# Kernel optimization log

Hardware: AMD Instinct MI355X
Metric: run time of the kernel (lower is better)

The kernel has to match this reference:

```python
import jax, jax.numpy as jnp
import numpy as np

P = 1.0  # Yager t-norm exponent (tnorm_p)


def _patches(x, k):
    # x: [B, C, H, W] -> [B, C*k*k, Ho, Wo], feature ordering (c, kh, kw) like torch unfold
    B, C, H, W = x.shape
    Ho, Wo = H - k + 1, W - k + 1
    cols = [x[:, :, i:i + Ho, j:j + Wo] for i in range(k) for j in range(k)]
    p = jnp.stack(cols, axis=2)  # [B, C, k*k, Ho, Wo]
    return p.reshape(B, C * k * k, Ho, Wo)


def _max_yager2d(x, w, p):
    # Fuzzy conv: Yager t-norm T(a,b)=max(0, 1-((1-a)^p+(1-b)^p)^(1/p)) between each
    # patch element and kernel weight, aggregated with max over the receptive field.
    O, C, k, _ = w.shape
    pat = _patches(x, k)                       # [B, L, Ho, Wo], L = C*k*k
    wf = w.reshape(O, -1)                      # [O, L]
    a = 1.0 - pat[:, None]                     # [B, 1, L, Ho, Wo]
    b = 1.0 - wf[None, :, :, None, None]       # [1, O, L, 1, 1]
    t = jnp.maximum(0.0, 1.0 - (a ** p + b ** p) ** (1.0 / p))
    return jnp.max(t, axis=2)                  # [B, O, Ho, Wo]


def _maxpool2(x):
    return jax.lax.reduce_window(x, -jnp.inf, jax.lax.max,
                                 (1, 1, 2, 2), (1, 1, 2, 2), 'VALID')


def setup_inputs() -> dict:
    key = jax.random.key(0)
    k1, k2, k3, k4, k5, k6, k7 = jax.random.split(key, 7)
    B = 128
    inputs = jax.random.uniform(k1, (B, 3, 32, 32), dtype=jnp.float32)
    # fuzzy kernels are membership values in [0,1]
    w1 = jax.random.uniform(k2, (6, 3, 5, 5), dtype=jnp.float32)
    w2 = jax.random.uniform(k3, (16, 6, 5, 5), dtype=jnp.float32)
    w3 = jax.random.uniform(k4, (120, 16, 5, 5), dtype=jnp.float32)
    wd = jax.random.normal(k5, (120, 84), dtype=jnp.float32) * 0.1  # DenseDefuzzy weights
    wf = jax.random.normal(k6, (84, 10), dtype=jnp.float32) * 0.1   # fc5 weight
    bf = jax.random.normal(k7, (10,), dtype=jnp.float32) * 0.01     # fc5 bias
    return {"inputs": inputs, "w1": w1, "w2": w2, "w3": w3,
            "wd": wd, "wf": wf, "bf": bf}


def reference(inputs, w1, w2, w3, wd, wf, bf):
    x = _maxpool2(_max_yager2d(inputs, w1, P))   # [B,6,14,14]
    x = _maxpool2(_max_yager2d(x, w2, P))        # [B,16,5,5]
    x = _max_yager2d(x, w3, P)                   # [B,120,1,1]
    x = x.reshape(x.shape[0], -1)                # [B,120]
    x = jnp.tanh(x @ wd)                         # DenseDefuzzy (unnormalized) + tanh
    return jax.nn.log_softmax(x @ wf + bf, axis=-1)
```

## Files before the change

kernel.cpp:

```cpp
#include <hip/hip_runtime.h>
#include <math.h>


#define NT 512
#define ROWS 34
#define PLANE (32 * ROWS)

__global__ __launch_bounds__(NT) void fused_lenet(
    const float* __restrict__ x,
    const float* __restrict__ w1,
    const float* __restrict__ w2,
    const float* __restrict__ w3,
    const float* __restrict__ wd,
    const float* __restrict__ wf,
    const float* __restrict__ bfv,
    float* __restrict__ out)
{
    const int img = blockIdx.x;
    const int tid = threadIdx.x;

    __shared__ float s_in[3 * PLANE];
    __shared__ float s_w1r[450];
    __shared__ float s_w2r[2400];
    __shared__ float s_w1d[648];
    __shared__ float s_w2d[3456];
    __shared__ unsigned s_a1u[1176];
    __shared__ unsigned s_a2u[400];
    __shared__ float s_a3[120];
    __shared__ float s_a4[84];

    {
        const float2* src = (const float2*)(x + img * 3072);
        for (int i = tid; i < 1536; i += NT) {
            const int c = i >> 9, rem = i & 511, r = rem >> 4, col2 = rem & 15;
            ((float2*)s_in)[c * (PLANE / 2) + r * (ROWS / 2) + col2] = src[i];
        }
        for (int i = tid; i < 225; i += NT)
            ((float2*)s_w1r)[i] = ((const float2*)w1)[i];
        for (int i = tid; i < 1200; i += NT)
            ((float2*)s_w2r)[i] = ((const float2*)w2)[i];
        for (int i = tid; i < 1176; i += NT) s_a1u[i] = 0u;
        if (tid < 400) s_a2u[tid] = 0u;
    }
    __syncthreads();

    for (int e = tid; e < 4104; e += NT) {
        const float* raw;
        float* dst;
        int v;
        if (e < 648) {
            const int oc = e / 108, u = e - oc * 108;
            const int c = u / 36; v = u - c * 36;
            raw = s_w1r + (oc * 3 + c) * 25;
            dst = s_w1d + e;
        } else {
            const int idx = e - 648;
            const int oc = idx / 216, u = idx - oc * 216;
            const int c = u / 36; v = u - c * 36;
            raw = s_w2r + (oc * 6 + c) * 25;
            dst = s_w2d + idx;
        }
        const int r = v / 6, col = v - r * 6;
        float m = -1e30f;
        #pragma unroll
        for (int dy = 0; dy < 2; ++dy) {
            const int kh = r - dy;
            if ((unsigned)kh > 4u) continue;
            #pragma unroll
            for (int dx = 0; dx < 2; ++dx) {
                const int kw = col - dx;
                if ((unsigned)kw > 4u) continue;
                m = fmaxf(m, raw[kh * 5 + kw]);
            }
        }
        *dst = m;
    }
    __syncthreads();

    if (tid < 504) {
        const int c = tid / 168;
        const int rr = tid - c * 168;
        const int oc = rr / 28;
        const int r2 = rr - oc * 28;
        const int py = r2 >> 1, s = r2 & 1;
        float acc[7];
        #pragma unroll
        for (int j = 0; j < 7; ++j) acc[j] = -1e30f;
        const float* wbase = s_w1d + (oc * 3 + c) * 36;
        #pragma unroll
        for (int uy = 0; uy < 6; ++uy) {
            const float* xr = s_in + c * PLANE + (2 * py + uy) * ROWS + 14 * s;
            float xv[18];
            #pragma unroll
            for (int i2 = 0; i2 < 9; ++i2)
                ((float2*)xv)[i2] = ((const float2*)xr)[i2];
            float wv[6];
            #pragma unroll
            for (int i2 = 0; i2 < 3; ++i2)
                ((float2*)wv)[i2] = ((const float2*)(wbase + uy * 6))[i2];
            #pragma unroll
            for (int j = 0; j < 7; ++j) {
                #pragma unroll
                for (int ux = 0; ux < 6; ++ux)
                    acc[j] = fmaxf(acc[j], xv[2 * j + ux] + wv[ux]);
            }
        }
        const int obase = oc * 196 + py * 14 + 7 * s;
        #pragma unroll
        for (int j = 0; j < 7; ++j) {
            const float rl = fmaxf(acc[j] - 1.0f, 0.0f);
            atomicMax(&s_a1u[obase + j], __float_as_uint(rl));
        }
    }
    __syncthreads();

    if (tid < 480) {
        const int oc = tid / 30;
        const int rr = tid - oc * 30;
        const int py = rr / 6;
        const int c = rr - py * 6;
        float acc[5];
        #pragma unroll
        for (int j = 0; j < 5; ++j) acc[j] = -1e30f;
        const float* a1f = (const float*)s_a1u;
        const float* wbase = s_w2d + (oc * 6 + c) * 36;
        #pragma unroll
        for (int uy = 0; uy < 6; ++uy) {
            const float* xr = a1f + c * 196 + (2 * py + uy) * 14;
            float xv[14];
            #pragma unroll
            for (int i2 = 0; i2 < 7; ++i2)
                ((float2*)xv)[i2] = ((const float2*)xr)[i2];
            float wv[6];
            #pragma unroll
            for (int i2 = 0; i2 < 3; ++i2)
                ((float2*)wv)[i2] = ((const float2*)(wbase + uy * 6))[i2];
            #pragma unroll
            for (int j = 0; j < 5; ++j) {
                #pragma unroll
                for (int ux = 0; ux < 6; ++ux)
                    acc[j] = fmaxf(acc[j], xv[2 * j + ux] + wv[ux]);
            }
        }
        const int obase = oc * 25 + py * 5;
        #pragma unroll
        for (int j = 0; j < 5; ++j) {
            const float rl = fmaxf(acc[j] - 1.0f, 0.0f);
            atomicMax(&s_a2u[obase + j], __float_as_uint(rl));
        }
    }
    __syncthreads();

    if (tid < 480) {
        const int o = tid >> 2, q = tid & 3;
        const float4* wv = (const float4*)(w3 + o * 400 + q * 100);
        const float4* av = (const float4*)((const float*)s_a2u + q * 100);
        float m = -1e30f;
        #pragma unroll 5
        for (int l = 0; l < 25; ++l) {
            const float4 w = wv[l];
            const float4 a = av[l];
            m = fmaxf(m, fmaxf(fmaxf(a.x + w.x, a.y + w.y),
                               fmaxf(a.z + w.z, a.w + w.w)));
        }
        m = fmaxf(m, __shfl_xor(m, 1));
        m = fmaxf(m, __shfl_xor(m, 2));
        if (q == 0) s_a3[o] = fmaxf(m - 1.0f, 0.0f);
    }
    __syncthreads();

    if (tid < 336) {
        const int o = tid >> 2, q = tid & 3;
        float acc = 0.0f;
        #pragma unroll 6
        for (int i = 0; i < 30; ++i) {
            const int k = q * 30 + i;
            acc = fmaf(s_a3[k], wd[k * 84 + o], acc);
        }
        acc += __shfl_xor(acc, 1);
        acc += __shfl_xor(acc, 2);
        if (q == 0) s_a4[o] = tanhf(acc);
    }
    __syncthreads();

    if (tid < 64) {
        float acc = 0.0f;
        if (tid < 40) {
            const int o = tid >> 2, q = tid & 3;
            #pragma unroll 7
            for (int i = 0; i < 21; ++i) {
                const int k = q * 21 + i;
                acc = fmaf(s_a4[k], wf[k * 10 + o], acc);
            }
            acc += __shfl_xor(acc, 1);
            acc += __shfl_xor(acc, 2);
            acc += bfv[o];
        }
        const float lg = __shfl(acc, (tid < 10) ? tid * 4 : 0);
        if (tid < 16) {
            float v = (tid < 10) ? lg : -1e30f;
            #pragma unroll
            for (int d = 1; d < 16; d <<= 1)
                v = fmaxf(v, __shfl_xor(v, d));
            float e = (tid < 10) ? expf(lg - v) : 0.0f;
            float ssum = e;
            #pragma unroll
            for (int d = 1; d < 16; d <<= 1)
                ssum += __shfl_xor(ssum, d);
            if (tid < 10)
                out[img * 10 + tid] = lg - v - logf(ssum);
        }
    }
}

extern "C" void kernel_launch(void* const* d_in, const int* in_sizes, int n_in,
                              void* d_out, int out_size, void* d_ws, size_t ws_size,
                              hipStream_t stream) {
    const float* x   = (const float*)d_in[0];
    const float* w1  = (const float*)d_in[1];
    const float* w2  = (const float*)d_in[2];
    const float* w3  = (const float*)d_in[3];
    const float* wd  = (const float*)d_in[4];
    const float* wf  = (const float*)d_in[5];
    const float* bfv = (const float*)d_in[6];
    float* out = (float*)d_out;

    const int B = in_sizes[0] / (3 * 32 * 32);
    fused_lenet<<<dim3(B), dim3(NT), 0, stream>>>(
        x, w1, w2, w3, wd, wf, bfv, out);
}
```

Before: 84.68 us.

## Double block size and split conv rows across thread halves, load weights directly

Raises threads per block from 512 to 1024. Conv1 and conv2 now split each dilated-weight window's six rows into two halves of three, handled by separate threads, and combine them through the existing shared-memory atomicMax. Conv3 and the dense layer split their reductions over 8 lanes instead of 4. The raw weights are read from global memory during dilation, which drops the staging copy and one barrier. The cost is more atomics and heavier register limits at 1024 threads, which may lower occupancy with only 128 blocks.

```diff
diff --git a/kernel.cpp b/kernel.cpp
--- a/kernel.cpp
+++ b/kernel.cpp
@@ -2,7 +2,7 @@
 #include <math.h>
 
 
-#define NT 512
+#define NT 1024
 #define ROWS 34
 #define PLANE (32 * ROWS)
 
@@ -20,8 +20,6 @@
     const int tid = threadIdx.x;
 
     __shared__ float s_in[3 * PLANE];
-    __shared__ float s_w1r[450];
-    __shared__ float s_w2r[2400];
     __shared__ float s_w1d[648];
     __shared__ float s_w2d[3456];
     __shared__ unsigned s_a1u[1176];
@@ -35,61 +33,59 @@
             const int c = i >> 9, rem = i & 511, r = rem >> 4, col2 = rem & 15;
             ((float2*)s_in)[c * (PLANE / 2) + r * (ROWS / 2) + col2] = src[i];
         }
-        for (int i = tid; i < 225; i += NT)
-            ((float2*)s_w1r)[i] = ((const float2*)w1)[i];
-        for (int i = tid; i < 1200; i += NT)
-            ((float2*)s_w2r)[i] = ((const float2*)w2)[i];
         for (int i = tid; i < 1176; i += NT) s_a1u[i] = 0u;
         if (tid < 400) s_a2u[tid] = 0u;
-    }
-    __syncthreads();
-
-    for (int e = tid; e < 4104; e += NT) {
-        const float* raw;
-        float* dst;
-        int v;
-        if (e < 648) {
-            const int oc = e / 108, u = e - oc * 108;
-            const int c = u / 36; v = u - c * 36;
-            raw = s_w1r + (oc * 3 + c) * 25;
-            dst = s_w1d + e;
-        } else {
-            const int idx = e - 648;
-            const int oc = idx / 216, u = idx - oc * 216;
-            const int c = u / 36; v = u - c * 36;
-            raw = s_w2r + (oc * 6 + c) * 25;
-            dst = s_w2d + idx;
-        }
-        const int r = v / 6, col = v - r * 6;
-        float m = -1e30f;
-        #pragma unroll
-        for (int dy = 0; dy < 2; ++dy) {
-            const int kh = r - dy;
-            if ((unsigned)kh > 4u) continue;
-            #pragma unroll
-            for (int dx = 0; dx < 2; ++dx) {
-                const int kw = col - dx;
-                if ((unsigned)kw > 4u) continue;
-                m = fmaxf(m, raw[kh * 5 + kw]);
-            }
-        }
-        *dst = m;
-    }
-    __syncthreads();
-
-    if (tid < 504) {
-        const int c = tid / 168;
-        const int rr = tid - c * 168;
-        const int oc = rr / 28;
-        const int r2 = rr - oc * 28;
-        const int py = r2 >> 1, s = r2 & 1;
+
+        for (int e = tid; e < 4104; e += NT) {
+            const float* raw;
+            float* dst;
+            int v;
+            if (e < 648) {
+                const int oc = e / 108, u = e - oc * 108;
+                const int c = u / 36; v = u - c * 36;
+                raw = w1 + (oc * 3 + c) * 25;
+                dst = s_w1d + e;
+            } else {
+                const int idx = e - 648;
+                const int oc = idx / 216, u = idx - oc * 216;
+                const int c = u / 36; v = u - c * 36;
+                raw = w2 + (oc * 6 + c) * 25;
+                dst = s_w2d + idx;
+            }
+            const int r = v / 6, col = v - r * 6;
+            float m = -1e30f;
+            #pragma unroll
+            for (int dy = 0; dy < 2; ++dy) {
+                const int kh = r - dy;
+                if ((unsigned)kh > 4u) continue;
+                #pragma unroll
+                for (int dx = 0; dx < 2; ++dx) {
+                    const int kw = col - dx;
+                    if ((unsigned)kw > 4u) continue;
+                    m = fmaxf(m, raw[kh * 5 + kw]);
+                }
+            }
+            *dst = m;
+        }
+    }
+    __syncthreads();
+
+    if (tid < 1008) {
+        const int c = tid / 336;
+        const int rr = tid - c * 336;
+        const int oc = rr / 56;
+        const int r2 = rr - oc * 56;
+        const int py = r2 >> 2;
+        const int s = (r2 >> 1) & 1;
+        const int h = r2 & 1;
         float acc[7];
         #pragma unroll
         for (int j = 0; j < 7; ++j) acc[j] = -1e30f;
-        const float* wbase = s_w1d + (oc * 3 + c) * 36;
-        #pragma unroll
-        for (int uy = 0; uy < 6; ++uy) {
-            const float* xr = s_in + c * PLANE + (2 * py + uy) * ROWS + 14 * s;
+        const float* wbase = s_w1d + (oc * 3 + c) * 36 + h * 18;
+        const float* xbase = s_in + c * PLANE + (2 * py + 3 * h) * ROWS + 14 * s;
+        #pragma unroll
+        for (int u = 0; u < 3; ++u) {
+            const float* xr = xbase + u * ROWS;
             float xv[18];
             #pragma unroll
             for (int i2 = 0; i2 < 9; ++i2)
@@ -97,7 +93,7 @@
             float wv[6];
             #pragma unroll
             for (int i2 = 0; i2 < 3; ++i2)
-                ((float2*)wv)[i2] = ((const float2*)(wbase + uy * 6))[i2];
+                ((float2*)wv)[i2] = ((const float2*)(wbase + u * 6))[i2];
             #pragma unroll
             for (int j = 0; j < 7; ++j) {
                 #pragma unroll
@@ -114,19 +110,22 @@
     }
     __syncthreads();
 
-    if (tid < 480) {
-        const int oc = tid / 30;
-        const int rr = tid - oc * 30;
-        const int py = rr / 6;
-        const int c = rr - py * 6;
+    if (tid < 960) {
+        const int oc = tid / 60;
+        const int rr = tid - oc * 60;
+        const int py = rr / 12;
+        const int r2 = rr - py * 12;
+        const int c = r2 >> 1;
+        const int h = r2 & 1;
         float acc[5];
         #pragma unroll
         for (int j = 0; j < 5; ++j) acc[j] = -1e30f;
         const float* a1f = (const float*)s_a1u;
-        const float* wbase = s_w2d + (oc * 6 + c) * 36;
-        #pragma unroll
-        for (int uy = 0; uy < 6; ++uy) {
-            const float* xr = a1f + c * 196 + (2 * py + uy) * 14;
+        const float* wbase = s_w2d + (oc * 6 + c) * 36 + h * 18;
+        const float* xbase = a1f + c * 196 + (2 * py + 3 * h) * 14;
+        #pragma unroll
+        for (int u = 0; u < 3; ++u) {
+            const float* xr = xbase + u * 14;
             float xv[14];
             #pragma unroll
             for (int i2 = 0; i2 < 7; ++i2)
@@ -134,7 +133,7 @@
             float wv[6];
             #pragma unroll
             for (int i2 = 0; i2 < 3; ++i2)
-                ((float2*)wv)[i2] = ((const float2*)(wbase + uy * 6))[i2];
+                ((float2*)wv)[i2] = ((const float2*)(wbase + u * 6))[i2];
             #pragma unroll
             for (int j = 0; j < 5; ++j) {
                 #pragma unroll
@@ -151,13 +150,12 @@
     }
     __syncthreads();
 
-    if (tid < 480) {
-        const int o = tid >> 2, q = tid & 3;
-        const float4* wv = (const float4*)(w3 + o * 400 + q * 100);
-        const float4* av = (const float4*)((const float*)s_a2u + q * 100);
+    if (tid < 960) {
+        const int o = tid >> 3, q = tid & 7;
+        const float4* wv = (const float4*)(w3 + o * 400);
+        const float4* av = (const float4*)(const float*)s_a2u;
         float m = -1e30f;
-        #pragma unroll 5
-        for (int l = 0; l < 25; ++l) {
+        for (int l = q; l < 100; l += 8) {
             const float4 w = wv[l];
             const float4 a = av[l];
             m = fmaxf(m, fmaxf(fmaxf(a.x + w.x, a.y + w.y),
@@ -165,20 +163,22 @@
         }
         m = fmaxf(m, __shfl_xor(m, 1));
         m = fmaxf(m, __shfl_xor(m, 2));
+        m = fmaxf(m, __shfl_xor(m, 4));
         if (q == 0) s_a3[o] = fmaxf(m - 1.0f, 0.0f);
     }
     __syncthreads();
 
-    if (tid < 336) {
-        const int o = tid >> 2, q = tid & 3;
+    if (tid < 672) {
+        const int o = tid >> 3, q = tid & 7;
         float acc = 0.0f;
-        #pragma unroll 6
-        for (int i = 0; i < 30; ++i) {
-            const int k = q * 30 + i;
+        #pragma unroll 5
+        for (int i = 0; i < 15; ++i) {
+            const int k = q * 15 + i;
             acc = fmaf(s_a3[k], wd[k * 84 + o], acc);
         }
         acc += __shfl_xor(acc, 1);
         acc += __shfl_xor(acc, 2);
+        acc += __shfl_xor(acc, 4);
         if (q == 0) s_a4[o] = tanhf(acc);
     }
     __syncthreads();
```

Result: faster. 81.91 us (-3.3%).
